# Performance work log

Hardware: AMD Instinct MI355X
Metric: run time of the kernel (lower is better)

The kernel has to match this reference:

```python
import jax, jax.numpy as jnp
import numpy as np

EPS = 1e-6
H = 8  # num_heads

def setup_inputs() -> dict:
    key = jax.random.key(0)
    ks = jax.random.split(key, 8)
    B, N, M, C, L = 4, 8192, 2048, 512, 256
    s = lambda f_in: 1.0 / np.sqrt(f_in)
    return {
        "input_tokens": jax.random.normal(ks[0], (B, N, C), jnp.float32),
        "query_tokens": jax.random.normal(ks[1], (B, M, C), jnp.float32),
        "Wq": jax.random.normal(ks[2], (C, L), jnp.float32) * s(C),
        "bq": jax.random.normal(ks[3], (L,), jnp.float32) * 0.01,
        "Wk": jax.random.normal(ks[4], (C, L), jnp.float32) * s(C),
        "bk": jax.random.normal(ks[5], (L,), jnp.float32) * 0.01,
        "Wv": jax.random.normal(ks[6], (C, C), jnp.float32) * s(C),
        "bv": jax.random.normal(ks[7], (C,), jnp.float32) * 0.01,
    }

def reference(input_tokens, query_tokens, Wq, bq, Wk, bk, Wv, bv):
    B, N, C = input_tokens.shape
    _, M, _ = query_tokens.shape
    L = Wq.shape[1]
    dL, dC = L // H, C // H
    # projections + head split
    q = (query_tokens @ Wq + bq).reshape(B, M, H, dL)
    k = (input_tokens @ Wk + bk).reshape(B, N, H, dL)
    v = (input_tokens @ Wv + bv).reshape(B, N, H, dC)
    # ELU+1 feature maps (positive kernel)
    q = jax.nn.elu(q) + 1.0
    k = jax.nn.elu(k) + 1.0
    # kv aggregation over input tokens: [B,H,dC,dL]
    kv = jnp.einsum('bnhd,bnhm->bhmd', k, v)
    # normalizer: q . sum_n k  -> [B,M,H]
    z = 1.0 / (jnp.einsum('bmhd,bhd->bmh', q, k.sum(axis=1)) + EPS)
    out = jnp.einsum('bmhd,bhcd,bmh->bmhc', q, kv, z)  # [B,M,H,dC]
    return out.reshape(B, M, C)
```

## Files before the change

kernel.cpp:

```cpp
#include <hip/hip_runtime.h>
#include <hip/hip_bf16.h>
#include <stdint.h>

typedef __bf16 bf16x8 __attribute__((ext_vector_type(8)));
typedef float f32x4 __attribute__((ext_vector_type(4)));

#define GLD16(gp, lp) __builtin_amdgcn_global_load_lds( \
    (__attribute__((address_space(1))) void*)(gp),      \
    (__attribute__((address_space(3))) void*)(lp), 16, 0, 0)

#define Bb 4
#define Nn 8192
#define Mm 2048
#define Cc 512
#define Ll 256
#define Hh 8
#define dLL 32
#define dCC 64
#define NTOK 32768

__global__ __launch_bounds__(256) void convert_bf16(
    const float* __restrict__ X, const float* __restrict__ Q,
    __hip_bfloat16* __restrict__ dst )
{
    const long NX = (long)Bb * Nn * Cc;
    const long NT = NX + (long)Bb * Mm * Cc;
    long i = ((long)blockIdx.x * 256 + threadIdx.x) * 8;
    if (i >= NT) return;
    const float* src; long off;
    if (i < NX) { src = X; off = i; } else { src = Q; off = i - NX; }
    float4 a = *(const float4*)(src + off);
    float4 b = *(const float4*)(src + off + 4);
    __hip_bfloat16 t8[8] = {
        __float2bfloat16(a.x), __float2bfloat16(a.y),
        __float2bfloat16(a.z), __float2bfloat16(a.w),
        __float2bfloat16(b.x), __float2bfloat16(b.y),
        __float2bfloat16(b.z), __float2bfloat16(b.w)};
    *(uint4*)(dst + i) = *(const uint4*)t8;
}

__global__ __launch_bounds__(256) void transpose_w(
    const float* __restrict__ Wk, const float* __restrict__ Wv,
    const float* __restrict__ Wq,
    __hip_bfloat16* __restrict__ Wkvt, __hip_bfloat16* __restrict__ Wqt)
{
    int idx = blockIdx.x * 256 + threadIdx.x;
    const int NKV = 768 * 512;
    if (idx < NKV) {
        int j = idx >> 9, c = idx & 511;
        float v = (j < 256) ? Wk[c * 256 + j] : Wv[c * 512 + (j - 256)];
        Wkvt[idx] = __float2bfloat16(v);
    } else {
        int k = idx - NKV;
        int j = k >> 9, c = k & 511;
        Wqt[k] = __float2bfloat16(Wq[c * 256 + j]);
    }
}

template<int MODE>
__global__ __launch_bounds__(256)
void gemm_bt(const __hip_bfloat16* __restrict__ A,
             const __hip_bfloat16* __restrict__ Bt,
             const float* __restrict__ bias0, const float* __restrict__ bias1,
             __hip_bfloat16* __restrict__ C,
             int Mdim, int Ndim, int Kdim)
{
    __shared__ __hip_bfloat16 lA[128 * 32];
    __shared__ __hip_bfloat16 lB[128 * 32];
    const int tid  = threadIdx.x;
    const int lane = tid & 63;
    const int wv   = tid >> 6;
    const int wm   = wv >> 1, wn = wv & 1;
    const long gm0 = (long)blockIdx.x * 128;
    const long gn0 = (long)blockIdx.y * 128;

    const int o0 = tid * 16;
    const int row0 = o0 >> 6;
    const int kb0 = o0 & 63;
    const int o1 = o0 + 4096;
    const int row1 = row0 + 64;
    const char* Apc = (const char*)A;
    const char* Bpc = (const char*)Bt;
    const long stride = (long)Kdim * 2;
    char* lApc = (char*)lA;
    char* lBpc = (char*)lB;

    f32x4 acc[4][4];
#pragma unroll
    for (int i = 0; i < 4; i++)
#pragma unroll
        for (int j = 0; j < 4; j++) acc[i][j] = (f32x4){0.f, 0.f, 0.f, 0.f};

    const int l16 = lane & 15, lq = lane >> 4;
    int aoff[4], boff[4];
#pragma unroll
    for (int i = 0; i < 4; i++) {
        aoff[i] = (wm * 64 + i * 16 + l16) * 64 + lq * 16;
        boff[i] = (wn * 64 + i * 16 + l16) * 64 + lq * 16;
    }

    const int KT = Kdim >> 5;
    for (int kt = 0; kt < KT; ++kt) {
        const long kbyte = (long)kt * 64;
        GLD16(Apc + (gm0 + row0) * stride + kbyte + kb0, lApc + o0);
        GLD16(Apc + (gm0 + row1) * stride + kbyte + kb0, lApc + o1);
        GLD16(Bpc + (gn0 + row0) * stride + kbyte + kb0, lBpc + o0);
        GLD16(Bpc + (gn0 + row1) * stride + kbyte + kb0, lBpc + o1);
        __syncthreads();
        bf16x8 af[4], bfr[4];
#pragma unroll
        for (int i = 0; i < 4; i++) af[i]  = *(const bf16x8*)(lApc + aoff[i]);
#pragma unroll
        for (int j = 0; j < 4; j++) bfr[j] = *(const bf16x8*)(lBpc + boff[j]);
#pragma unroll
        for (int i = 0; i < 4; i++)
#pragma unroll
            for (int j = 0; j < 4; j++)
                acc[i][j] = __builtin_amdgcn_mfma_f32_16x16x32_bf16(
                    af[i], bfr[j], acc[i][j], 0, 0, 0);
        __syncthreads();
    }

#pragma unroll
    for (int i = 0; i < 4; i++) {
        const long gmr = gm0 + wm * 64 + i * 16 + lq * 4;
#pragma unroll
        for (int j = 0; j < 4; j++) {
            const int gn = (int)gn0 + wn * 64 + j * 16 + l16;
            float bias;
            bool act;
            if (MODE == 0) {
                act = (gn < 256);
                bias = act ? bias0[gn] : bias1[gn - 256];
            } else {
                act = true;
                bias = bias0[gn];
            }
            if (MODE == 0) {
                __hip_bfloat16 o4[4];
#pragma unroll
                for (int v = 0; v < 4; v++) {
                    float x = acc[i][j][v] + bias;
                    if (act) x = (x > 0.f) ? x + 1.f : __expf(x);
                    o4[v] = __float2bfloat16(x);
                }
                *(ushort4*)(&C[(long)gn * Mdim + gmr]) = *(const ushort4*)o4;
            } else {
#pragma unroll
                for (int v = 0; v < 4; v++) {
                    float x = acc[i][j][v] + bias;
                    x = (x > 0.f) ? x + 1.f : __expf(x);
                    C[(gmr + v) * (long)Ndim + gn] = __float2bfloat16(x);
                }
            }
        }
    }
}

__global__ __launch_bounds__(256)
void kv_mfma(const __hip_bfloat16* __restrict__ kvT, float* __restrict__ kvpart)
{
    __shared__ char lds[2][12288];
    const int chunk = blockIdx.x, h = blockIdx.y, b = blockIdx.z;
    const int t = threadIdx.x;
    const long RS = (long)NTOK * 2;
    const long tokB0 = (long)b * (Nn * 2) + chunk * 1024;
    const char* kc = (const char*)kvT;
    const int r = t >> 3;
    const int wsw = ((t * 16) & 127) ^ ((r & 7) << 4);
    const char* pK  = kc + (h * 32 + r) * RS + tokB0 + wsw;
    const char* pV0 = kc + (256 + h * 64 + r) * RS + tokB0 + wsw;
    const char* pV1 = pV0 + 32 * RS;

    const int w = t >> 6, l16 = t & 15, lq = (t >> 4) & 3;
    const int arow = w * 16 + l16;
    int aoffs[2], boffs[2][2];
#pragma unroll
    for (int ks = 0; ks < 2; ++ks) {
        const int wb = ks * 64 + lq * 16;
        aoffs[ks] = arow * 128 + (wb ^ ((arow & 7) << 4));
        boffs[ks][0] = l16 * 128 + (wb ^ ((l16 & 7) << 4));
        boffs[ks][1] = boffs[ks][0] + 2048;
    }

    f32x4 acc0 = {0.f, 0.f, 0.f, 0.f}, acc1 = {0.f, 0.f, 0.f, 0.f};

    {
        char* bf = lds[0];
        GLD16(pK,  bf + t * 16);
        GLD16(pV0, bf + 4096 + t * 16);
        GLD16(pV1, bf + 8192 + t * 16);
    }
    __syncthreads();
    int cur = 0;
    for (int kt = 0; kt < 8; ++kt) {
        if (kt < 7) {
            char* bf = lds[cur ^ 1];
            const long kb = (long)(kt + 1) * 128;
            GLD16(pK + kb,  bf + t * 16);
            GLD16(pV0 + kb, bf + 4096 + t * 16);
            GLD16(pV1 + kb, bf + 8192 + t * 16);
        }
        const char* lK = lds[cur];
        const char* lV = lds[cur] + 4096;
#pragma unroll
        for (int ks = 0; ks < 2; ++ks) {
            bf16x8 av = *(const bf16x8*)(lV + aoffs[ks]);
            bf16x8 b0 = *(const bf16x8*)(lK + boffs[ks][0]);
            bf16x8 b1 = *(const bf16x8*)(lK + boffs[ks][1]);
            acc0 = __builtin_amdgcn_mfma_f32_16x16x32_bf16(av, b0, acc0, 0, 0, 0);
            acc1 = __builtin_amdgcn_mfma_f32_16x16x32_bf16(av, b1, acc1, 0, 0, 0);
        }
        __syncthreads();
        cur ^= 1;
    }

    float* op = kvpart + (((long)(b * 8 + h) * 16 + chunk) * 2048);
#pragma unroll
    for (int v = 0; v < 4; ++v) {
        const int c = w * 16 + lq * 4 + v;
        op[c * 32 + l16]      = acc0[v];
        op[c * 32 + 16 + l16] = acc1[v];
    }
}

__global__ __launch_bounds__(256)
void reduce_kv(const float* __restrict__ part, float* __restrict__ kvagg)
{
    int idx = blockIdx.x * 256 + threadIdx.x;
    int bh = idx >> 11, cd = idx & 2047;
    const float* p = part + (long)bh * 16 * 2048 + cd;
    float s = 0.f;
#pragma unroll
    for (int ch = 0; ch < 16; ++ch) s += p[ch * 2048];
    kvagg[idx] = s;
}

__global__ __launch_bounds__(256)
void ksum_kernel(const __hip_bfloat16* __restrict__ kvT, float* __restrict__ ksum)
{
    const int j = blockIdx.x;
    const int b = blockIdx.y;
    const int t = threadIdx.x;
    const __hip_bfloat16* row = kvT + (long)j * NTOK + b * Nn + t * 32;
    float s = 0.f;
#pragma unroll
    for (int u = 0; u < 4; ++u) {
        bf16x8 kv8 = *(const bf16x8*)(row + u * 8);
#pragma unroll
        for (int e = 0; e < 8; ++e) s += (float)kv8[e];
    }
    __shared__ float red[256];
    red[t] = s;
    __syncthreads();
    for (int st = 128; st > 0; st >>= 1) {
        if (t < st) red[t] += red[t + st];
        __syncthreads();
    }
    if (t == 0) ksum[b * 256 + j] = red[0];
}

__global__ __launch_bounds__(256)
void z_kernel(const __hip_bfloat16* __restrict__ qb,
              const float* __restrict__ ksum, float* __restrict__ zb)
{
    int t = blockIdx.x * 256 + threadIdx.x;
    int m = t >> 3, h = t & 7;
    int b = m >> 11;
    const __hip_bfloat16* q = qb + (long)m * 256 + h * 32;
    const float* ks = ksum + ((long)b * Hh + h) * 32;
    float s = 0.f;
#pragma unroll
    for (int d8 = 0; d8 < 4; ++d8) {
        bf16x8 qv = *(const bf16x8*)(q + d8 * 8);
#pragma unroll
        for (int u = 0; u < 8; ++u) s = fmaf((float)qv[u], ks[d8 * 8 + u], s);
    }
    zb[t] = 1.f / (s + 1e-6f);
}

__global__ __launch_bounds__(256)
void out_kernel(const __hip_bfloat16* __restrict__ qb,
                const float* __restrict__ kvagg, const float* __restrict__ zb,
                float* __restrict__ out)
{
    __shared__ float lqf[32 * 256];
    __shared__ float lz[32 * 8];
    const int b = blockIdx.y, mt = blockIdx.x;
    const int t = threadIdx.x;
    const long qrow0 = (long)b * Mm + mt * 32;

#pragma unroll
    for (int r = 0; r < 4; ++r) {
        int e = (r * 256 + t) * 8;
        bf16x8 qv = *(const bf16x8*)(qb + qrow0 * 256 + e);
        f32x4 lo = {(float)qv[0], (float)qv[1], (float)qv[2], (float)qv[3]};
        f32x4 hi = {(float)qv[4], (float)qv[5], (float)qv[6], (float)qv[7]};
        *(f32x4*)&lqf[e] = lo;
        *(f32x4*)&lqf[e + 4] = hi;
    }
    lz[t & 255] = zb[qrow0 * 8 + (t & 255)];

    float kv0[32], kv1[32];
    const float* kvb = kvagg + (long)b * (Hh * 64 * 32);
#pragma unroll
    for (int d4 = 0; d4 < 8; ++d4) {
        *(f32x4*)&kv0[d4 * 4] = *(const f32x4*)&kvb[(long)t * 32 + d4 * 4];
        *(f32x4*)&kv1[d4 * 4] = *(const f32x4*)&kvb[((long)t + 256) * 32 + d4 * 4];
    }
    __syncthreads();

    const int h0 = t >> 6;
    for (int r = 0; r < 32; ++r) {
        float a0 = 0.f, a1 = 0.f;
        const float* q0 = &lqf[r * 256 + h0 * 32];
        const float* q1 = q0 + 128;
#pragma unroll
        for (int d = 0; d < 32; ++d) {
            a0 = fmaf(q0[d], kv0[d], a0);
            a1 = fmaf(q1[d], kv1[d], a1);
        }
        const float z0 = lz[r * 8 + h0];
        const float z1 = lz[r * 8 + h0 + 4];
        const long ob = (qrow0 + r) * 512;
        out[ob + t] = a0 * z0;
        out[ob + t + 256] = a1 * z1;
    }
}

extern "C" void kernel_launch(void* const* d_in, const int* in_sizes, int n_in,
                              void* d_out, int out_size, void* d_ws, size_t ws_size,
                              hipStream_t stream)
{
    const float* X  = (const float*)d_in[0];
    const float* Qt = (const float*)d_in[1];
    const float* Wq = (const float*)d_in[2];
    const float* bq = (const float*)d_in[3];
    const float* Wk = (const float*)d_in[4];
    const float* bk = (const float*)d_in[5];
    const float* Wv = (const float*)d_in[6];
    const float* bv = (const float*)d_in[7];
    float* out = (float*)d_out;

    __hip_bfloat16* Xb    = (__hip_bfloat16*)d_ws;
    __hip_bfloat16* Qb    = Xb + (long)32768 * 512;
    __hip_bfloat16* Wkvt  = Qb + (long)8192 * 512;
    __hip_bfloat16* Wqt   = Wkvt + 768 * 512;
    __hip_bfloat16* kvT   = Wqt + 256 * 512;
    __hip_bfloat16* qbuf  = kvT + (long)768 * NTOK;
    float* kvagg = (float*)(qbuf + (long)8192 * 256);
    float* ksum  = kvagg + 4 * 8 * 64 * 32;
    float* zbuf  = ksum + 4 * 256;
    float* kvpart = (float*)d_ws;

    convert_bf16<<<10240, 256, 0, stream>>>(X, Qt, Xb);
    transpose_w<<<2048, 256, 0, stream>>>(Wk, Wv, Wq, Wkvt, Wqt);
    gemm_bt<0><<<dim3(256, 6), 256, 0, stream>>>(Xb, Wkvt, bk, bv, kvT, 32768, 768, 512);
    gemm_bt<1><<<dim3(64, 2), 256, 0, stream>>>(Qb, Wqt, bq, nullptr, qbuf, 8192, 256, 512);
    kv_mfma<<<dim3(16, 8, 4), 256, 0, stream>>>(kvT, kvpart);
    ksum_kernel<<<dim3(256, 4), 256, 0, stream>>>(kvT, ksum);
    reduce_kv<<<256, 256, 0, stream>>>(kvpart, kvagg);
    z_kernel<<<256, 256, 0, stream>>>(qbuf, ksum, zbuf);
    out_kernel<<<dim3(64, 4), 256, 0, stream>>>(qbuf, kvagg, zbuf, out);
}
```

Before: 219.7 us.

## Reassociate V projection: contract X^T K first, then apply Wv

Instead of projecting all input tokens through Wv and then aggregating K^T V, the code computes X^T K per batch with a split-K MFMA GEMM, reduces the partials, and contracts the result with Wv while adding the bias term via ksum. This removes the large token-level V projection and its intermediate storage. It adds a transposed bf16 copy of X and extra reduction kernels. The GEMM also gains double-buffered LDS prefetch.

```diff
diff --git a/kernel.cpp b/kernel.cpp
--- a/kernel.cpp
+++ b/kernel.cpp
@@ -15,58 +15,80 @@
 #define Cc 512
 #define Ll 256
 #define Hh 8
-#define dLL 32
-#define dCC 64
 #define NTOK 32768
 
-__global__ __launch_bounds__(256) void convert_bf16(
-    const float* __restrict__ X, const float* __restrict__ Q,
-    __hip_bfloat16* __restrict__ dst )
-{
-    const long NX = (long)Bb * Nn * Cc;
-    const long NT = NX + (long)Bb * Mm * Cc;
+__global__ __launch_bounds__(256) void convert_q(
+    const float* __restrict__ Q, __hip_bfloat16* __restrict__ Qb)
+{
     long i = ((long)blockIdx.x * 256 + threadIdx.x) * 8;
-    if (i >= NT) return;
-    const float* src; long off;
-    if (i < NX) { src = X; off = i; } else { src = Q; off = i - NX; }
-    float4 a = *(const float4*)(src + off);
-    float4 b = *(const float4*)(src + off + 4);
+    float4 a = *(const float4*)(Q + i);
+    float4 b = *(const float4*)(Q + i + 4);
     __hip_bfloat16 t8[8] = {
         __float2bfloat16(a.x), __float2bfloat16(a.y),
         __float2bfloat16(a.z), __float2bfloat16(a.w),
         __float2bfloat16(b.x), __float2bfloat16(b.y),
         __float2bfloat16(b.z), __float2bfloat16(b.w)};
-    *(uint4*)(dst + i) = *(const uint4*)t8;
-}
-
-__global__ __launch_bounds__(256) void transpose_w(
-    const float* __restrict__ Wk, const float* __restrict__ Wv,
-    const float* __restrict__ Wq,
-    __hip_bfloat16* __restrict__ Wkvt, __hip_bfloat16* __restrict__ Wqt)
+    *(uint4*)(Qb + i) = *(const uint4*)t8;
+}
+
+__global__ __launch_bounds__(256) void transpose_x(
+    const float* __restrict__ X,
+    __hip_bfloat16* __restrict__ Xb, __hip_bfloat16* __restrict__ XbT)
+{
+    __shared__ __hip_bfloat16 ldsT[64][72];
+    const int tn = blockIdx.x, tc = blockIdx.y;
+    const long n0 = (long)tn * 64;
+    const int c0 = tc * 64;
+    const int t = threadIdx.x;
+    const int rl = t >> 4;
+    const int c4 = (t & 15) * 4;
+#pragma unroll
+    for (int u = 0; u < 4; ++u) {
+        const int row = rl + u * 16;
+        f32x4 a = *(const f32x4*)(X + (n0 + row) * Cc + c0 + c4);
+        __hip_bfloat16 b4[4] = {
+            __float2bfloat16(a.x), __float2bfloat16(a.y),
+            __float2bfloat16(a.z), __float2bfloat16(a.w)};
+        *(ushort2*)(&Xb[(n0 + row) * Cc + c0 + c4]) = *(const ushort2*)b4;
+        *(ushort2*)(&Xb[(n0 + row) * Cc + c0 + c4 + 2]) = *(const ushort2*)(b4 + 2);
+#pragma unroll
+        for (int i = 0; i < 4; ++i) ldsT[c4 + i][row] = b4[i];
+    }
+    __syncthreads();
+#pragma unroll
+    for (int u = 0; u < 2; ++u) {
+        const int v = u * 256 + t;
+        const int orow = v >> 3;
+        const int oc8 = (v & 7) * 8;
+        bf16x8 r = *(const bf16x8*)(&ldsT[orow][oc8]);
+        *(bf16x8*)(&XbT[(long)(c0 + orow) * NTOK + n0 + oc8]) = r;
+    }
+}
+
+__global__ __launch_bounds__(256) void transpose_w2(
+    const float* __restrict__ Wk, const float* __restrict__ Wq,
+    __hip_bfloat16* __restrict__ WkT, __hip_bfloat16* __restrict__ WqT)
 {
     int idx = blockIdx.x * 256 + threadIdx.x;
-    const int NKV = 768 * 512;
-    if (idx < NKV) {
+    const int NK = 256 * 512;
+    if (idx < NK) {
         int j = idx >> 9, c = idx & 511;
-        float v = (j < 256) ? Wk[c * 256 + j] : Wv[c * 512 + (j - 256)];
-        Wkvt[idx] = __float2bfloat16(v);
+        WkT[idx] = __float2bfloat16(Wk[c * 256 + j]);
     } else {
-        int k = idx - NKV;
+        int k = idx - NK;
         int j = k >> 9, c = k & 511;
-        Wqt[k] = __float2bfloat16(Wq[c * 256 + j]);
+        WqT[k] = __float2bfloat16(Wq[c * 256 + j]);
     }
 }
 
 template<int MODE>
 __global__ __launch_bounds__(256)
-void gemm_bt(const __hip_bfloat16* __restrict__ A,
-             const __hip_bfloat16* __restrict__ Bt,
-             const float* __restrict__ bias0, const float* __restrict__ bias1,
-             __hip_bfloat16* __restrict__ C,
-             int Mdim, int Ndim, int Kdim)
-{
-    __shared__ __hip_bfloat16 lA[128 * 32];
-    __shared__ __hip_bfloat16 lB[128 * 32];
+void gemm_bt(const __hip_bfloat16* __restrict__ A, long lda,
+             const __hip_bfloat16* __restrict__ Bt, long ldb,
+             const float* __restrict__ bias,
+             void* __restrict__ Cout, long ldc, int Klen)
+{
+    __shared__ char lds[2][16384];
     const int tid  = threadIdx.x;
     const int lane = tid & 63;
     const int wv   = tid >> 6;
@@ -74,16 +96,22 @@
     const long gm0 = (long)blockIdx.x * 128;
     const long gn0 = (long)blockIdx.y * 128;
 
+    long koff_el = 0;
+    if (MODE == 2) {
+        const int z = blockIdx.z;
+        koff_el = (long)(z >> 3) * Nn + (long)(z & 7) * 1024;
+    }
+
     const int o0 = tid * 16;
     const int row0 = o0 >> 6;
     const int kb0 = o0 & 63;
     const int o1 = o0 + 4096;
     const int row1 = row0 + 64;
-    const char* Apc = (const char*)A;
-    const char* Bpc = (const char*)Bt;
-    const long stride = (long)Kdim * 2;
-    char* lApc = (char*)lA;
-    char* lBpc = (char*)lB;
+    const long sA = lda * 2, sB = ldb * 2;
+    const char* pA0 = (const char*)A + (gm0 + row0) * sA + koff_el * 2 + kb0;
+    const char* pA1 = (const char*)A + (gm0 + row1) * sA + koff_el * 2 + kb0;
+    const char* pB0 = (const char*)Bt + (gn0 + row0) * sB + koff_el * 2 + kb0;
+    const char* pB1 = (const char*)Bt + (gn0 + row1) * sB + koff_el * 2 + kb0;
 
     f32x4 acc[4][4];
 #pragma unroll
@@ -96,22 +124,30 @@
 #pragma unroll
     for (int i = 0; i < 4; i++) {
         aoff[i] = (wm * 64 + i * 16 + l16) * 64 + lq * 16;
-        boff[i] = (wn * 64 + i * 16 + l16) * 64 + lq * 16;
-    }
-
-    const int KT = Kdim >> 5;
+        boff[i] = 8192 + (wn * 64 + i * 16 + l16) * 64 + lq * 16;
+    }
+
+    const int KT = Klen >> 5;
+    {
+        char* bf = lds[0];
+        GLD16(pA0, bf + o0); GLD16(pA1, bf + o1);
+        GLD16(pB0, bf + 8192 + o0); GLD16(pB1, bf + 8192 + o1);
+    }
+    __syncthreads();
     for (int kt = 0; kt < KT; ++kt) {
-        const long kbyte = (long)kt * 64;
-        GLD16(Apc + (gm0 + row0) * stride + kbyte + kb0, lApc + o0);
-        GLD16(Apc + (gm0 + row1) * stride + kbyte + kb0, lApc + o1);
-        GLD16(Bpc + (gn0 + row0) * stride + kbyte + kb0, lBpc + o0);
-        GLD16(Bpc + (gn0 + row1) * stride + kbyte + kb0, lBpc + o1);
-        __syncthreads();
+        const int cur = kt & 1;
+        if (kt + 1 < KT) {
+            char* bf = lds[cur ^ 1];
+            const long kb = (long)(kt + 1) * 64;
+            GLD16(pA0 + kb, bf + o0); GLD16(pA1 + kb, bf + o1);
+            GLD16(pB0 + kb, bf + 8192 + o0); GLD16(pB1 + kb, bf + 8192 + o1);
+        }
+        const char* lp = lds[cur];
         bf16x8 af[4], bfr[4];
 #pragma unroll
-        for (int i = 0; i < 4; i++) af[i]  = *(const bf16x8*)(lApc + aoff[i]);
-#pragma unroll
-        for (int j = 0; j < 4; j++) bfr[j] = *(const bf16x8*)(lBpc + boff[j]);
+        for (int i = 0; i < 4; i++) af[i]  = *(const bf16x8*)(lp + aoff[i]);
+#pragma unroll
+        for (int j = 0; j < 4; j++) bfr[j] = *(const bf16x8*)(lp + boff[j]);
 #pragma unroll
         for (int i = 0; i < 4; i++)
 #pragma unroll
@@ -121,36 +157,28 @@
         __syncthreads();
     }
 
+    __hip_bfloat16* Cb = (__hip_bfloat16*)Cout;
+    float* Cf = (float*)Cout;
+    if (MODE == 2) Cf += (long)blockIdx.z * (512 * 256);
 #pragma unroll
     for (int i = 0; i < 4; i++) {
         const long gmr = gm0 + wm * 64 + i * 16 + lq * 4;
 #pragma unroll
         for (int j = 0; j < 4; j++) {
             const int gn = (int)gn0 + wn * 64 + j * 16 + l16;
-            float bias;
-            bool act;
-            if (MODE == 0) {
-                act = (gn < 256);
-                bias = act ? bias0[gn] : bias1[gn - 256];
-            } else {
-                act = true;
-                bias = bias0[gn];
-            }
-            if (MODE == 0) {
-                __hip_bfloat16 o4[4];
-#pragma unroll
-                for (int v = 0; v < 4; v++) {
-                    float x = acc[i][j][v] + bias;
-                    if (act) x = (x > 0.f) ? x + 1.f : __expf(x);
-                    o4[v] = __float2bfloat16(x);
-                }
-                *(ushort4*)(&C[(long)gn * Mdim + gmr]) = *(const ushort4*)o4;
-            } else {
-#pragma unroll
-                for (int v = 0; v < 4; v++) {
-                    float x = acc[i][j][v] + bias;
+#pragma unroll
+            for (int v = 0; v < 4; v++) {
+                float x = acc[i][j][v];
+                if (MODE == 0) {
+                    x += bias[gmr + v];
                     x = (x > 0.f) ? x + 1.f : __expf(x);
-                    C[(gmr + v) * (long)Ndim + gn] = __float2bfloat16(x);
+                    Cb[(gmr + v) * ldc + gn] = __float2bfloat16(x);
+                } else if (MODE == 1) {
+                    x += bias[gn];
+                    x = (x > 0.f) ? x + 1.f : __expf(x);
+                    Cb[(gmr + v) * ldc + gn] = __float2bfloat16(x);
+                } else {
+                    Cf[(gmr + v) * ldc + gn] = x;
                 }
             }
         }
@@ -158,91 +186,12 @@
 }
 
 __global__ __launch_bounds__(256)
-void kv_mfma(const __hip_bfloat16* __restrict__ kvT, float* __restrict__ kvpart)
-{
-    __shared__ char lds[2][12288];
-    const int chunk = blockIdx.x, h = blockIdx.y, b = blockIdx.z;
-    const int t = threadIdx.x;
-    const long RS = (long)NTOK * 2;
-    const long tokB0 = (long)b * (Nn * 2) + chunk * 1024;
-    const char* kc = (const char*)kvT;
-    const int r = t >> 3;
-    const int wsw = ((t * 16) & 127) ^ ((r & 7) << 4);
-    const char* pK  = kc + (h * 32 + r) * RS + tokB0 + wsw;
-    const char* pV0 = kc + (256 + h * 64 + r) * RS + tokB0 + wsw;
-    const char* pV1 = pV0 + 32 * RS;
-
-    const int w = t >> 6, l16 = t & 15, lq = (t >> 4) & 3;
-    const int arow = w * 16 + l16;
-    int aoffs[2], boffs[2][2];
-#pragma unroll
-    for (int ks = 0; ks < 2; ++ks) {
-        const int wb = ks * 64 + lq * 16;
-        aoffs[ks] = arow * 128 + (wb ^ ((arow & 7) << 4));
-        boffs[ks][0] = l16 * 128 + (wb ^ ((l16 & 7) << 4));
-        boffs[ks][1] = boffs[ks][0] + 2048;
-    }
-
-    f32x4 acc0 = {0.f, 0.f, 0.f, 0.f}, acc1 = {0.f, 0.f, 0.f, 0.f};
-
-    {
-        char* bf = lds[0];
-        GLD16(pK,  bf + t * 16);
-        GLD16(pV0, bf + 4096 + t * 16);
-        GLD16(pV1, bf + 8192 + t * 16);
-    }
-    __syncthreads();
-    int cur = 0;
-    for (int kt = 0; kt < 8; ++kt) {
-        if (kt < 7) {
-            char* bf = lds[cur ^ 1];
-            const long kb = (long)(kt + 1) * 128;
-            GLD16(pK + kb,  bf + t * 16);
-            GLD16(pV0 + kb, bf + 4096 + t * 16);
-            GLD16(pV1 + kb, bf + 8192 + t * 16);
-        }
-        const char* lK = lds[cur];
-        const char* lV = lds[cur] + 4096;
-#pragma unroll
-        for (int ks = 0; ks < 2; ++ks) {
-            bf16x8 av = *(const bf16x8*)(lV + aoffs[ks]);
-            bf16x8 b0 = *(const bf16x8*)(lK + boffs[ks][0]);
-            bf16x8 b1 = *(const bf16x8*)(lK + boffs[ks][1]);
-            acc0 = __builtin_amdgcn_mfma_f32_16x16x32_bf16(av, b0, acc0, 0, 0, 0);
-            acc1 = __builtin_amdgcn_mfma_f32_16x16x32_bf16(av, b1, acc1, 0, 0, 0);
-        }
-        __syncthreads();
-        cur ^= 1;
-    }
-
-    float* op = kvpart + (((long)(b * 8 + h) * 16 + chunk) * 2048);
-#pragma unroll
-    for (int v = 0; v < 4; ++v) {
-        const int c = w * 16 + lq * 4 + v;
-        op[c * 32 + l16]      = acc0[v];
-        op[c * 32 + 16 + l16] = acc1[v];
-    }
-}
-
-__global__ __launch_bounds__(256)
-void reduce_kv(const float* __restrict__ part, float* __restrict__ kvagg)
-{
-    int idx = blockIdx.x * 256 + threadIdx.x;
-    int bh = idx >> 11, cd = idx & 2047;
-    const float* p = part + (long)bh * 16 * 2048 + cd;
-    float s = 0.f;
-#pragma unroll
-    for (int ch = 0; ch < 16; ++ch) s += p[ch * 2048];
-    kvagg[idx] = s;
-}
-
-__global__ __launch_bounds__(256)
-void ksum_kernel(const __hip_bfloat16* __restrict__ kvT, float* __restrict__ ksum)
+void ksum_kernel(const __hip_bfloat16* __restrict__ kT, float* __restrict__ ksum)
 {
     const int j = blockIdx.x;
     const int b = blockIdx.y;
     const int t = threadIdx.x;
-    const __hip_bfloat16* row = kvT + (long)j * NTOK + b * Nn + t * 32;
+    const __hip_bfloat16* row = kT + (long)j * NTOK + b * Nn + t * 32;
     float s = 0.f;
 #pragma unroll
     for (int u = 0; u < 4; ++u) {
@@ -258,6 +207,56 @@
         __syncthreads();
     }
     if (t == 0) ksum[b * 256 + j] = red[0];
+}
+
+__global__ __launch_bounds__(256)
+void reduce_xk(const float* __restrict__ part, float* __restrict__ xk)
+{
+    int idx = blockIdx.x * 256 + threadIdx.x;
+    int b = idx >> 17, r = idx & 131071;
+    const float* p = part + (long)b * 8 * 131072 + r;
+    float s = 0.f;
+#pragma unroll
+    for (int ks = 0; ks < 8; ++ks) s += p[(long)ks * 131072];
+    xk[idx] = s;
+}
+
+__global__ __launch_bounds__(256)
+void wv_contract(const float* __restrict__ xk, const float* __restrict__ Wv,
+                 const float* __restrict__ bv, const float* __restrict__ ksum,
+                 float* __restrict__ kvagg)
+{
+    __shared__ float xs[512][32];
+    const int chg = blockIdx.x;
+    const int b = blockIdx.y;
+    const int t = threadIdx.x;
+    const int ch0 = chg * 16;
+    const int h = ch0 >> 6;
+    const float* xb = xk + (long)b * 131072 + h * 32;
+#pragma unroll
+    for (int u = 0; u < 16; ++u) {
+        const int v = u * 256 + t;
+        const int row = v >> 3, c4 = (v & 7) * 4;
+        *(f32x4*)&xs[row][c4] = *(const f32x4*)&xb[(long)row * 256 + c4];
+    }
+    __syncthreads();
+    const int ch_l = t >> 4;
+    const int d0 = (t & 15) * 2;
+    const int ch = ch0 + ch_l;
+    float a0 = 0.f, a1 = 0.f;
+#pragma unroll 8
+    for (int c = 0; c < 512; ++c) {
+        const float w = Wv[(long)c * 512 + ch];
+        a0 = fmaf(w, xs[c][d0], a0);
+        a1 = fmaf(w, xs[c][d0 + 1], a1);
+    }
+    const float bvv = bv[ch];
+    const float* ks = ksum + b * 256 + h * 32;
+    a0 += bvv * ks[d0];
+    a1 += bvv * ks[d0 + 1];
+    float* op = kvagg + (((long)(b * 8 + h) * 64 + (ch & 63)) * 32);
+    op[d0] = a0;
+    op[d0 + 1] = a1;
 }
 
 __global__ __launch_bounds__(256)
@@ -299,7 +298,7 @@
         *(f32x4*)&lqf[e] = lo;
         *(f32x4*)&lqf[e + 4] = hi;
     }
-    lz[t & 255] = zb[qrow0 * 8 + (t & 255)];
+    lz[t] = zb[qrow0 * 8 + t];
 
     float kv0[32], kv1[32];
     const float* kvb = kvagg + (long)b * (Hh * 64 * 32);
@@ -343,23 +342,27 @@
     float* out = (float*)d_out;
 
     __hip_bfloat16* Xb    = (__hip_bfloat16*)d_ws;
-    __hip_bfloat16* Qb    = Xb + (long)32768 * 512;
-    __hip_bfloat16* Wkvt  = Qb + (long)8192 * 512;
-    __hip_bfloat16* Wqt   = Wkvt + 768 * 512;
-    __hip_bfloat16* kvT   = Wqt + 256 * 512;
-    __hip_bfloat16* qbuf  = kvT + (long)768 * NTOK;
-    float* kvagg = (float*)(qbuf + (long)8192 * 256);
+    __hip_bfloat16* Qb    = Xb + (long)NTOK * Cc;
+    __hip_bfloat16* XbT   = Qb + (long)8192 * Cc;
+    __hip_bfloat16* kT    = XbT + (long)Cc * NTOK;
+    __hip_bfloat16* WkT   = kT + (long)Ll * NTOK;
+    __hip_bfloat16* WqT   = WkT + 256 * 512;
+    __hip_bfloat16* qbuf  = WqT + 256 * 512;
+    float* xk    = (float*)(qbuf + (long)8192 * 256);
+    float* kvagg = xk + (long)4 * 512 * 256;
     float* ksum  = kvagg + 4 * 8 * 64 * 32;
     float* zbuf  = ksum + 4 * 256;
-    float* kvpart = (float*)d_ws;
-
-    convert_bf16<<<10240, 256, 0, stream>>>(X, Qt, Xb);
-    transpose_w<<<2048, 256, 0, stream>>>(Wk, Wv, Wq, Wkvt, Wqt);
-    gemm_bt<0><<<dim3(256, 6), 256, 0, stream>>>(Xb, Wkvt, bk, bv, kvT, 32768, 768, 512);
-    gemm_bt<1><<<dim3(64, 2), 256, 0, stream>>>(Qb, Wqt, bq, nullptr, qbuf, 8192, 256, 512);
-    kv_mfma<<<dim3(16, 8, 4), 256, 0, stream>>>(kvT, kvpart);
-    ksum_kernel<<<dim3(256, 4), 256, 0, stream>>>(kvT, ksum);
-    reduce_kv<<<256, 256, 0, stream>>>(kvpart, kvagg);
+    float* xkpart = (float*)d_ws;
+
+    convert_q<<<2048, 256, 0, stream>>>(Qt, Qb);
+    transpose_x<<<dim3(512, 8), 256, 0, stream>>>(X, Xb, XbT);
+    transpose_w2<<<1024, 256, 0, stream>>>(Wk, Wq, WkT, WqT);
+    gemm_bt<0><<<dim3(2, 256), 256, 0, stream>>>(WkT, 512, Xb, 512, bk, kT, NTOK, 512);
+    gemm_bt<1><<<dim3(64, 2), 256, 0, stream>>>(Qb, 512, WqT, 512, bq, qbuf, 256, 512);
+    ksum_kernel<<<dim3(256, 4), 256, 0, stream>>>(kT, ksum);
+    gemm_bt<2><<<dim3(4, 2, 32), 256, 0, stream>>>(XbT, NTOK, kT, NTOK, nullptr, xkpart, 256, 1024);
+    reduce_xk<<<2048, 256, 0, stream>>>(xkpart, xk);
+    wv_contract<<<dim3(32, 4), 256, 0, stream>>>(xk, Wv, bv, ksum, kvagg);
     z_kernel<<<256, 256, 0, stream>>>(qbuf, ksum, zbuf);
     out_kernel<<<dim3(64, 4), 256, 0, stream>>>(qbuf, kvagg, zbuf, out);
 }
```

Result: slower. 241.3 us (+9.8%).
